# Performance work log

Measured on AMD Instinct MI355X. Metric: run time of the kernel, lower is better.

Reference implementation:

```python
import jax, jax.numpy as jnp
import numpy as np

B, C, H, W = 32, 1, 28, 896
WW = WS = 28
S = (W - WW) // WS + 1  # 32 windows
CONV_DIM, FC_DIM, NUM_CLASSES = 64, 128, 83
FC_IN = CONV_DIM * (H // 2) * (WW // 2)  # 64*14*14 = 12544


def setup_inputs() -> dict:
    key = jax.random.key(0)
    ks = jax.random.split(key, 9)
    sc = 0.05
    return {
        "x": jax.random.normal(ks[0], (B, C, H, W), jnp.float32),
        "conv1_w": jax.random.normal(ks[1], (CONV_DIM, C, 3, 3), jnp.float32) * sc,
        "conv1_b": jax.random.normal(ks[2], (CONV_DIM,), jnp.float32) * sc,
        "conv2_w": jax.random.normal(ks[3], (CONV_DIM, CONV_DIM, 3, 3), jnp.float32) * sc,
        "conv2_b": jax.random.normal(ks[4], (CONV_DIM,), jnp.float32) * sc,
        "fc1_w": jax.random.normal(ks[5], (FC_DIM, FC_IN), jnp.float32) * sc,
        "fc1_b": jax.random.normal(ks[6], (FC_DIM,), jnp.float32) * sc,
        "fc2_w": jax.random.normal(ks[7], (NUM_CLASSES, FC_DIM), jnp.float32) * sc,
        "fc2_b": jax.random.normal(ks[8], (NUM_CLASSES,), jnp.float32) * sc,
    }


def _conv_relu(x, w, b):
    # 3x3 conv, stride 1, padding 1 (torch Conv2d padding=1), then ReLU
    y = jax.lax.conv_general_dilated(
        x, w, window_strides=(1, 1), padding=((1, 1), (1, 1)),
        dimension_numbers=("NCHW", "OIHW", "NCHW"))
    return jax.nn.relu(y + b[None, :, None, None])


def reference(x, conv1_w, conv1_b, conv2_w, conv2_b, fc1_w, fc1_b, fc2_w, fc2_b):
    Bx = x.shape[0]
    # WS == WW -> non-overlapping windows; extract all S windows at once via reshape
    # (B, C, H, S*WW) -> (B*S, C, H, WW)
    win = x.reshape(Bx, C, H, S, WW).transpose(0, 3, 1, 2, 4).reshape(Bx * S, C, H, WW)
    h = _conv_relu(win, conv1_w, conv1_b)
    h = _conv_relu(h, conv2_w, conv2_b)
    # MaxPool2d(2)
    h = jax.lax.reduce_window(h, -jnp.inf, jax.lax.max,
                              window_dimensions=(1, 1, 2, 2),
                              window_strides=(1, 1, 2, 2), padding="VALID")
    # dropout is identity in eval mode
    h = h.reshape(Bx * S, FC_IN)  # torch.flatten(x, 1) on NCHW matches row-major reshape
    h = jax.nn.relu(h @ fc1_w.T + fc1_b)
    logits = h @ fc2_w.T + fc2_b  # (B*S, num_classes)
    # -> (B, num_classes, S) as in the torch module
    return logits.reshape(Bx, S, NUM_CLASSES).transpose(0, 2, 1)
```

## Files before the change

### kernel.cpp

```cpp
#include <hip/hip_runtime.h>
#include <hip/hip_bf16.h>


typedef __attribute__((ext_vector_type(8))) short short8;
typedef __attribute__((ext_vector_type(4))) float f32x4;

#define WB1_E   0u
#define WB2_E   2048u
#define WFC1_E  38912u
#define WFC2_E  1644544u
#define POOL_E  1656832u
#define PART_B  29003776u

__device__ __forceinline__ unsigned short f2bf(float f) {
  unsigned u = __float_as_uint(f);
  u += 0x7fffu + ((u >> 16) & 1u);
  return (unsigned short)(u >> 16);
}

__global__ __launch_bounds__(256) void prep_kernel(
    const float* __restrict__ w1, const float* __restrict__ c1b,
    const float* __restrict__ w2, const float* __restrict__ wfc1,
    const float* __restrict__ wfc2, unsigned short* __restrict__ ws16)
{
  int i = blockIdx.x * blockDim.x + threadIdx.x;
  if (i < 2048) {
    int j = i & 7, l = (i >> 3) & 63, nt = i >> 9;
    int n = nt * 16 + (l & 15), k = 8 * (l >> 4) + j;
    float v = (k < 9) ? w1[n * 9 + k] : (k == 9 ? c1b[n] : 0.f);
    ws16[WB1_E + i] = f2bf(v);
  } else if (i < 38912) {
    int i2 = i - 2048;
    int j = i2 & 7, l = (i2 >> 3) & 63, rest = i2 >> 9;
    int ks = rest % 18, nt = rest / 18;
    int n = nt * 16 + (l & 15);
    int kk = ks * 32 + 8 * (l >> 4) + j;
    int dydx = kk >> 6, ci = kk & 63;
    ws16[WB2_E + i2] = f2bf(w2[n * 576 + ci * 9 + dydx]);
  } else if (i < 1644544) {
    int i2 = i - 38912;
    int j = i2 & 7, l = (i2 >> 3) & 63, rest = i2 >> 9;
    int ks = rest % 392, nt = rest / 392;
    int fcn = nt * 16 + (l & 15);
    int kp = ks * 32 + 8 * (l >> 4) + j;
    int co = kp & 63, r2 = kp >> 6;
    int oxp = r2 % 14, oyp = r2 / 14;
    ws16[WFC1_E + i2] = f2bf(wfc1[fcn * 12544 + co * 196 + oyp * 14 + oxp]);
  } else if (i < 1656832) {
    int i2 = i - 1644544;
    int j = i2 & 7, l = (i2 >> 3) & 63, rest = i2 >> 9;
    int ks = rest & 3, nt = rest >> 2;
    int cls = nt * 16 + (l & 15);
    int k = ks * 32 + 8 * (l >> 4) + j;
    float v = (cls < 83) ? wfc2[cls * 128 + k] : 0.f;
    ws16[WFC2_E + i2] = f2bf(v);
  }
}

__global__ __launch_bounds__(512, 4) void conv_kernel(
    const float* __restrict__ x, const float* __restrict__ c2b,
    unsigned short* __restrict__ ws16)
{
  extern __shared__ char smem[];
  unsigned short* xw = (unsigned short*)(smem + 77760);

  const int tid = threadIdx.x;
  const int wave = tid >> 6, lane = tid & 63;
  const int g = lane >> 4, l15 = lane & 15;
  const int bid = blockIdx.x;
  const int n = bid >> 1, hf = bid & 1;
  const int rlo = hf ? 15 : 0;
  const int M1 = hf ? 364 : 476;
  const int T1 = hf ? 23 : 30;
  const int T2 = hf ? 21 : 28;
  const int lr_off = hf ? -15 : 1;

  const short8* wb1 = (const short8*)(ws16 + WB1_E);
  const short8* wb2 = (const short8*)(ws16 + WB2_E);
  unsigned short* poolg = ws16 + POOL_E + (unsigned)n * 12544u;

  short8 z8 = {0, 0, 0, 0, 0, 0, 0, 0};
  {
    short8* l8 = (short8*)smem;
    for (int idx = tid; idx < 4860; idx += 512) l8[idx] = z8;
    const float* xg = x + (n >> 5) * 25088 + (n & 31) * 28;
    for (int i = tid; i < 900; i += 512) {
      int yy = (i * 2185) >> 16;
      int xx = i - yy * 30;
      int iy = yy - 1, ix = xx - 1;
      bool inb = (iy >= 0) && (iy < 28) && (ix >= 0) && (ix < 28);
      float v = inb ? xg[iy * 896 + ix] : 0.f;
      xw[i] = f2bf(v);
    }
  }
  __syncthreads();

  {
    short8 b1f[4];
#pragma unroll
    for (int nt = 0; nt < 4; ++nt) b1f[nt] = wb1[nt * 64 + lane];
    for (int mt = wave; mt < T1; mt += 8) {
      int m = mt * 16 + l15;
      bool mval = m < M1;
      int mc = mval ? m : M1 - 1;
      int yr = (mc * 2341) >> 16;
      int rr = rlo + yr;
      int ox = mc - yr * 28;
      const char* xb = (const char*)xw + (rr * 30 + ox) * 2;
      short8 a = z8;
      if (g == 0) {
        a[0] = *(const short*)(xb + 0);
        a[1] = *(const short*)(xb + 2);
        a[2] = *(const short*)(xb + 4);
        a[3] = *(const short*)(xb + 60);
        a[4] = *(const short*)(xb + 62);
        a[5] = *(const short*)(xb + 64);
        a[6] = *(const short*)(xb + 120);
        a[7] = *(const short*)(xb + 122);
      } else if (g == 1) {
        a[0] = *(const short*)(xb + 124);
        a[1] = (short)0x3F80;
      }
      f32x4 d[4];
#pragma unroll
      for (int nt = 0; nt < 4; ++nt) {
        f32x4 zz = {0.f, 0.f, 0.f, 0.f};
        d[nt] = __builtin_amdgcn_mfma_f32_16x16x32_bf16(b1f[nt], a, zz, 0, 0, 0);
      }
      if (mval) {
        int spB = ((rr + lr_off) * 30 + ox + 1) * 144;
#pragma unroll
        for (int nt = 0; nt < 4; ++nt)
#pragma unroll
          for (int t = 0; t < 2; ++t) {
            int co2 = nt * 16 + 4 * g + 2 * t;
            unsigned pk = (unsigned)f2bf(fmaxf(d[nt][2 * t], 0.f)) |
                          ((unsigned)f2bf(fmaxf(d[nt][2 * t + 1], 0.f)) << 16);
            *(unsigned*)(smem + (spB + co2 * 2)) = pk;
          }
      }
    }
  }
  __syncthreads();

  {
    const int ntp = (wave < 4) ? 0 : 2;
    const int mg = wave & 3;
    float c2bv[2];
#pragma unroll
    for (int tn = 0; tn < 2; ++tn) c2bv[tn] = c2b[(ntp + tn) * 16 + l15];
    const int w4 = l15 >> 2;
    const int oyw = 2 * (w4 >> 1) + ((l15 >> 1) & 1);
    const int oxw = 2 * (w4 & 1) + (l15 & 1);
    int baseB[7];
#pragma unroll
    for (int mi = 0; mi < 7; ++mi) {
      int mt = mg + 4 * mi;
      int ryy = (mt * 37) >> 8;
      int rx = mt - 7 * ryy;
      baseB[mi] = ((4 * ryy + oyw) * 30 + 4 * rx + oxw) * 144 + 16 * g;
    }
    f32x4 acc[7][2];
#pragma unroll
    for (int mi = 0; mi < 7; ++mi) {
      f32x4 zz = {0.f, 0.f, 0.f, 0.f};
      acc[mi][0] = zz; acc[mi][1] = zz;
    }
#pragma unroll 1
    for (int phase = 0; phase < 6; ++phase) {
      short8 bfr[2][3];
#pragma unroll
      for (int tn = 0; tn < 2; ++tn)
#pragma unroll
        for (int ks = 0; ks < 3; ++ks)
          bfr[tn][ks] = wb2[((ntp + tn) * 18 + phase * 3 + ks) * 64 + lane];
      int dspB[3];
#pragma unroll
      for (int ks = 0; ks < 3; ++ks) {
        int ksg = phase * 3 + ks;
        int dydx = ksg >> 1;
        int dy = (dydx * 11) >> 5;
        int dx = dydx - 3 * dy;
        dspB[ks] = (dy * 30 + dx) * 144 + ((ksg & 1) << 6);
      }
#pragma unroll
      for (int mi = 0; mi < 7; ++mi) {
        int mt = mg + 4 * mi;
        if (mt < T2) {
#pragma unroll
          for (int ks = 0; ks < 3; ++ks) {
            short8 a = *(const short8*)(smem + (baseB[mi] + dspB[ks]));
            acc[mi][0] = __builtin_amdgcn_mfma_f32_16x16x32_bf16(a, bfr[0][ks], acc[mi][0], 0, 0, 0);
            acc[mi][1] = __builtin_amdgcn_mfma_f32_16x16x32_bf16(a, bfr[1][ks], acc[mi][1], 0, 0, 0);
          }
        }
      }
    }
    const int yb = hf ? 8 : 0;
#pragma unroll
    for (int mi = 0; mi < 7; ++mi) {
      int mt = mg + 4 * mi;
      if (mt < T2) {
        int ryy = (mt * 37) >> 8;
        int rx = mt - 7 * ryy;
        int oyp = yb + 2 * ryy + (g >> 1);
        int oxp = 2 * rx + (g & 1);
#pragma unroll
        for (int tn = 0; tn < 2; ++tn) {
          int co = (ntp + tn) * 16 + l15;
          f32x4 v = acc[mi][tn];
          float p = fmaxf(fmaxf(v[0], v[1]), fmaxf(v[2], v[3]));
          p = fmaxf(p + c2bv[tn], 0.f);
          poolg[(oyp * 14 + oxp) * 64 + co] = f2bf(p);
        }
      }
    }
  }
}

__global__ __launch_bounds__(512) void fc1_kernel(unsigned short* __restrict__ ws16)
{
  extern __shared__ char smem[];
  short8* A8 = (short8*)smem;
  const int tid = threadIdx.x;
  const int wave = tid >> 6, lane = tid & 63;
  const int g = lane >> 4, l15 = lane & 15;
  const int ig = blockIdx.x >> 2, q = blockIdx.x & 3;
  const short8* pool8 = (const short8*)(ws16 + POOL_E);
  const short8* wf1 = (const short8*)(ws16 + WFC1_E);
  {
    int img = tid >> 5, l32 = tid & 31;
    const short8* src = pool8 + (ig * 16 + img) * 1568 + q * 392;
#pragma unroll
    for (int j = 0; j < 13; ++j) {
      int idx = l32 + 32 * j;
      if (idx < 392) A8[img * 393 + idx] = src[idx];
    }
  }
  __syncthreads();
  f32x4 acc = {0.f, 0.f, 0.f, 0.f};
  const short8* wbase = wf1 + (wave * 392 + q * 98) * 64 + lane;
#pragma unroll 2
  for (int ks = 0; ks < 98; ++ks) {
    short8 b = wbase[ks * 64];
    short8 a = A8[l15 * 393 + ks * 4 + g];
    acc = __builtin_amdgcn_mfma_f32_16x16x32_bf16(a, b, acc, 0, 0, 0);
  }
  _Float16* part = (_Float16*)((char*)ws16 + PART_B);
  int base = ((q * 64 + ig) * 16 + 4 * g) * 128 + wave * 16 + l15;
#pragma unroll
  for (int i = 0; i < 4; ++i) part[base + i * 128] = (_Float16)acc[i];
}

__global__ __launch_bounds__(512) void fc2_kernel(
    const float* __restrict__ b1, const float* __restrict__ b2,
    const unsigned short* __restrict__ ws16, float* __restrict__ out)
{
  __shared__ unsigned short h_s[16 * 136];
  const int tid = threadIdx.x;
  const int wave = tid >> 6, lane = tid & 63;
  const int g = lane >> 4, l15 = lane & 15;
  const int ig = blockIdx.x;
  const _Float16* part = (const _Float16*)((const char*)ws16 + PART_B);
#pragma unroll
  for (int t = 0; t < 4; ++t) {
    int u = tid + 512 * t;
    int img = u >> 7, fcn = u & 127;
    float s = 0.f;
#pragma unroll
    for (int q2 = 0; q2 < 4; ++q2)
      s += (float)part[((q2 * 64 + ig) * 16 + img) * 128 + fcn];
    h_s[img * 136 + fcn] = f2bf(fmaxf(s + b1[fcn], 0.f));
  }
  __syncthreads();
  if (wave < 6) {
    const short8* wf2 = (const short8*)(ws16 + WFC2_E);
    const short8* h8 = (const short8*)h_s;
    f32x4 a2 = {0.f, 0.f, 0.f, 0.f};
#pragma unroll
    for (int ks = 0; ks < 4; ++ks) {
      short8 b = wf2[(wave * 4 + ks) * 64 + lane];
      short8 a = h8[l15 * 17 + ks * 4 + g];
      a2 = __builtin_amdgcn_mfma_f32_16x16x32_bf16(a, b, a2, 0, 0, 0);
    }
    int cls = wave * 16 + l15;
    if (cls < 83) {
      float bias2 = b2[cls];
#pragma unroll
      for (int i = 0; i < 4; ++i) {
        int nimg = ig * 16 + 4 * g + i;
        out[((nimg >> 5) * 83 + cls) * 32 + (nimg & 31)] = a2[i] + bias2;
      }
    }
  }
}

extern "C" void kernel_launch(void* const* d_in, const int* in_sizes, int n_in,
                              void* d_out, int out_size, void* d_ws, size_t ws_size,
                              hipStream_t stream)
{
  const float* x    = (const float*)d_in[0];
  const float* w1   = (const float*)d_in[1];
  const float* c1b  = (const float*)d_in[2];
  const float* w2   = (const float*)d_in[3];
  const float* c2b  = (const float*)d_in[4];
  const float* wfc1 = (const float*)d_in[5];
  const float* bfc1 = (const float*)d_in[6];
  const float* wfc2 = (const float*)d_in[7];
  const float* bfc2 = (const float*)d_in[8];
  unsigned short* ws16 = (unsigned short*)d_ws;
  float* out = (float*)d_out;

  prep_kernel<<<6472, 256, 0, stream>>>(w1, c1b, w2, wfc1, wfc2, ws16);
  conv_kernel<<<2048, 512, 79616, stream>>>(x, c2b, ws16);
  fc1_kernel<<<256, 512, 100608, stream>>>(ws16);
  fc2_kernel<<<64, 512, 0, stream>>>(bfc1, bfc2, ws16, out);
}
```

Baseline: 98.23 us.

## Switch conv2 to 32x32x16 MFMA tiles and split fc1 accumulator chain

Conv2 now uses the 32x32x16 bf16 MFMA. Each wave covers 32 output channels and 32 pooled-quad pixels per tile, with weights repacked into a matching layout in the prep kernel and the phase loop fully unrolled over the nine taps. This aims to cut LDS A-fragment loads per FLOP and the per-instruction overhead compared with the 16x16 tiles. The fc1 loop alternates between two accumulators to break the serial MFMA dependency chain. The cost is a larger register footprint, 64 accumulator floats per wave-tile, which could lower occupancy.

Result: no change. 100.0 us (+1.8%).

```diff
diff --git a/kernel.cpp b/kernel.cpp
--- a/kernel.cpp
+++ b/kernel.cpp
@@ -4,6 +4,7 @@
 
 typedef __attribute__((ext_vector_type(8))) short short8;
 typedef __attribute__((ext_vector_type(4))) float f32x4;
+typedef __attribute__((ext_vector_type(16))) float f32x16;
 
 #define WB1_E   0u
 #define WB2_E   2048u
@@ -32,11 +33,11 @@
   } else if (i < 38912) {
     int i2 = i - 2048;
     int j = i2 & 7, l = (i2 >> 3) & 63, rest = i2 >> 9;
-    int ks = rest % 18, nt = rest / 18;
-    int n = nt * 16 + (l & 15);
-    int kk = ks * 32 + 8 * (l >> 4) + j;
-    int dydx = kk >> 6, ci = kk & 63;
-    ws16[WB2_E + i2] = f2bf(w2[n * 576 + ci * 9 + dydx]);
+    int ks = rest % 36, nh = rest / 36;
+    int co = nh * 32 + (l & 31);
+    int k = ks * 16 + (l >> 5) * 8 + j;
+    int dydx = k >> 6, ci = k & 63;
+    ws16[WB2_E + i2] = f2bf(w2[co * 576 + ci * 9 + dydx]);
   } else if (i < 1644544) {
     int i2 = i - 38912;
     int j = i2 & 7, l = (i2 >> 3) & 63, rest = i2 >> 9;
@@ -66,17 +67,14 @@
 
   const int tid = threadIdx.x;
   const int wave = tid >> 6, lane = tid & 63;
-  const int g = lane >> 4, l15 = lane & 15;
   const int bid = blockIdx.x;
   const int n = bid >> 1, hf = bid & 1;
   const int rlo = hf ? 15 : 0;
   const int M1 = hf ? 364 : 476;
   const int T1 = hf ? 23 : 30;
-  const int T2 = hf ? 21 : 28;
   const int lr_off = hf ? -15 : 1;
 
   const short8* wb1 = (const short8*)(ws16 + WB1_E);
-  const short8* wb2 = (const short8*)(ws16 + WB2_E);
   unsigned short* poolg = ws16 + POOL_E + (unsigned)n * 12544u;
 
   short8 z8 = {0, 0, 0, 0, 0, 0, 0, 0};
@@ -96,6 +94,7 @@
   __syncthreads();
 
   {
+    const int g = lane >> 4, l15 = lane & 15;
     short8 b1f[4];
 #pragma unroll
     for (int nt = 0; nt < 4; ++nt) b1f[nt] = wb1[nt * 64 + lane];
@@ -144,74 +143,59 @@
   __syncthreads();
 
   {
-    const int ntp = (wave < 4) ? 0 : 2;
-    const int mg = wave & 3;
-    float c2bv[2];
-#pragma unroll
-    for (int tn = 0; tn < 2; ++tn) c2bv[tn] = c2b[(ntp + tn) * 16 + l15];
-    const int w4 = l15 >> 2;
-    const int oyw = 2 * (w4 >> 1) + ((l15 >> 1) & 1);
-    const int oxw = 2 * (w4 & 1) + (l15 & 1);
-    int baseB[7];
-#pragma unroll
-    for (int mi = 0; mi < 7; ++mi) {
-      int mt = mg + 4 * mi;
-      int ryy = (mt * 37) >> 8;
-      int rx = mt - 7 * ryy;
-      baseB[mi] = ((4 * ryy + oyw) * 30 + 4 * rx + oxw) * 144 + 16 * g;
-    }
-    f32x4 acc[7][2];
-#pragma unroll
-    for (int mi = 0; mi < 7; ++mi) {
-      f32x4 zz = {0.f, 0.f, 0.f, 0.f};
-      acc[mi][0] = zz; acc[mi][1] = zz;
-    }
-#pragma unroll 1
-    for (int phase = 0; phase < 6; ++phase) {
-      short8 bfr[2][3];
-#pragma unroll
-      for (int tn = 0; tn < 2; ++tn)
-#pragma unroll
-        for (int ks = 0; ks < 3; ++ks)
-          bfr[tn][ks] = wb2[((ntp + tn) * 18 + phase * 3 + ks) * 64 + lane];
-      int dspB[3];
-#pragma unroll
-      for (int ks = 0; ks < 3; ++ks) {
-        int ksg = phase * 3 + ks;
-        int dydx = ksg >> 1;
-        int dy = (dydx * 11) >> 5;
-        int dx = dydx - 3 * dy;
-        dspB[ks] = (dy * 30 + dx) * 144 + ((ksg & 1) << 6);
-      }
-#pragma unroll
-      for (int mi = 0; mi < 7; ++mi) {
-        int mt = mg + 4 * mi;
-        if (mt < T2) {
-#pragma unroll
-          for (int ks = 0; ks < 3; ++ks) {
-            short8 a = *(const short8*)(smem + (baseB[mi] + dspB[ks]));
-            acc[mi][0] = __builtin_amdgcn_mfma_f32_16x16x32_bf16(a, bfr[0][ks], acc[mi][0], 0, 0, 0);
-            acc[mi][1] = __builtin_amdgcn_mfma_f32_16x16x32_bf16(a, bfr[1][ks], acc[mi][1], 0, 0, 0);
+    const int nh = wave >> 2;
+    const int wg = wave & 3;
+    const int l31 = lane & 31;
+    const int h = lane >> 5;
+    const int T32 = hf ? 11 : 14;
+    const int Wh  = hf ? 84 : 112;
+    const float bias = c2b[nh * 32 + l31];
+    const short8* wb2w = (const short8*)(ws16 + WB2_E) + nh * 2304 + lane;
+
+    int baseB[4];
+#pragma unroll
+    for (int t = 0; t < 4; ++t) {
+      int tI = wg + 4 * t;
+      int lw = tI * 8 + (l31 >> 2);
+      int py = lw / 14, px = lw % 14;
+      int R = 2 * py + ((l31 >> 1) & 1);
+      int C = 2 * px + (l31 & 1);
+      baseB[t] = (R * 30 + C) * 144 + h * 16;
+    }
+    f32x16 acc[4];
+#pragma unroll
+    for (int t = 0; t < 4; ++t) acc[t] = (f32x16)(0.0f);
+
+#pragma unroll
+    for (int ph = 0; ph < 9; ++ph) {
+      const int cellO = ((ph / 3) * 30 + (ph % 3)) * 144;
+      short8 bf[4];
+#pragma unroll
+      for (int ksb = 0; ksb < 4; ++ksb) bf[ksb] = wb2w[(ph * 4 + ksb) * 64];
+#pragma unroll
+      for (int t = 0; t < 4; ++t) {
+        if (wg + 4 * t < T32) {
+#pragma unroll
+          for (int ksb = 0; ksb < 4; ++ksb) {
+            short8 a = *(const short8*)(smem + (baseB[t] + (cellO + 32 * ksb)));
+            acc[t] = __builtin_amdgcn_mfma_f32_32x32x16_bf16(a, bf[ksb], acc[t], 0, 0, 0);
           }
         }
       }
     }
-    const int yb = hf ? 8 : 0;
-#pragma unroll
-    for (int mi = 0; mi < 7; ++mi) {
-      int mt = mg + 4 * mi;
-      if (mt < T2) {
-        int ryy = (mt * 37) >> 8;
-        int rx = mt - 7 * ryy;
-        int oyp = yb + 2 * ryy + (g >> 1);
-        int oxp = 2 * rx + (g & 1);
-#pragma unroll
-        for (int tn = 0; tn < 2; ++tn) {
-          int co = (ntp + tn) * 16 + l15;
-          f32x4 v = acc[mi][tn];
-          float p = fmaxf(fmaxf(v[0], v[1]), fmaxf(v[2], v[3]));
-          p = fmaxf(p + c2bv[tn], 0.f);
-          poolg[(oyp * 14 + oxp) * 64 + co] = f2bf(p);
+#pragma unroll
+    for (int t = 0; t < 4; ++t) {
+      int tI = wg + 4 * t;
+      if (tI < T32) {
+#pragma unroll
+        for (int q = 0; q < 4; ++q) {
+          int lw = tI * 8 + 2 * q + h;
+          if (lw < Wh) {
+            float p = fmaxf(fmaxf(acc[t][4 * q + 0], acc[t][4 * q + 1]),
+                            fmaxf(acc[t][4 * q + 2], acc[t][4 * q + 3]));
+            p = fmaxf(p + bias, 0.f);
+            poolg[(hf * 112 + lw) * 64 + nh * 32 + l31] = f2bf(p);
+          }
         }
       }
     }
@@ -238,18 +222,19 @@
     }
   }
   __syncthreads();
-  f32x4 acc = {0.f, 0.f, 0.f, 0.f};
+  f32x4 accA = {0.f, 0.f, 0.f, 0.f}, accB = {0.f, 0.f, 0.f, 0.f};
   const short8* wbase = wf1 + (wave * 392 + q * 98) * 64 + lane;
 #pragma unroll 2
   for (int ks = 0; ks < 98; ++ks) {
     short8 b = wbase[ks * 64];
     short8 a = A8[l15 * 393 + ks * 4 + g];
-    acc = __builtin_amdgcn_mfma_f32_16x16x32_bf16(a, b, acc, 0, 0, 0);
+    if (ks & 1) accB = __builtin_amdgcn_mfma_f32_16x16x32_bf16(a, b, accB, 0, 0, 0);
+    else        accA = __builtin_amdgcn_mfma_f32_16x16x32_bf16(a, b, accA, 0, 0, 0);
   }
   _Float16* part = (_Float16*)((char*)ws16 + PART_B);
   int base = ((q * 64 + ig) * 16 + 4 * g) * 128 + wave * 16 + l15;
 #pragma unroll
-  for (int i = 0; i < 4; ++i) part[base + i * 128] = (_Float16)acc[i];
+  for (int i = 0; i < 4; ++i) part[base + i * 128] = (_Float16)(accA[i] + accB[i]);
 }
 
 __global__ __launch_bounds__(512) void fc2_kernel(
```
